# Kernel tuning notes

Hardware: AMD Instinct MI355X
Metric: run time of the kernel (lower is better)

Reference implementation:

```python
import jax, jax.numpy as jnp
import numpy as np

L, R, C = 4, 4, 32          # corr_levels, corr_radius, corr_channels
D = 2 * R + 1               # 9 displacements per axis
B, H, W = 2, 48, 64         # feature resolution (1/8 of a 384x512 image)


def _conv(x, w, b, stride=1, pad=1):
    out = jax.lax.conv_general_dilated(x, w, (stride, stride), [(pad, pad), (pad, pad)],
                                       dimension_numbers=('NCHW', 'OIHW', 'NCHW'))
    return out + b[None, :, None, None]


def _deconv(x, w, b):
    # ConvTranspose2d(k=4, s=2, p=1) as lhs-dilated conv with edge padding k-1-p = 2
    out = jax.lax.conv_general_dilated(x, w, (1, 1), [(2, 2), (2, 2)],
                                       lhs_dilation=(2, 2),
                                       dimension_numbers=('NCHW', 'OIHW', 'NCHW'))
    return out + b[None, :, None, None]


def _grid_sample(img, grid):
    # bilinear, align_corners=True, zero padding; img [B,C,H,W], grid [B,Hg,Wg,2] in [-1,1]
    Bn, Ch, Hi, Wi = img.shape
    gx = (grid[..., 0] + 1.0) * 0.5 * (Wi - 1)
    gy = (grid[..., 1] + 1.0) * 0.5 * (Hi - 1)
    x0 = jnp.floor(gx); y0 = jnp.floor(gy)
    wx = gx - x0; wy = gy - y0
    def corner(xi, yi, wgt):
        valid = (xi >= 0) & (xi <= Wi - 1) & (yi >= 0) & (yi <= Hi - 1)
        xc = jnp.clip(xi, 0, Wi - 1).astype(jnp.int32)
        yc = jnp.clip(yi, 0, Hi - 1).astype(jnp.int32)
        v = jax.vmap(lambda im, y, x: im[:, y, x])(img, yc, xc)  # [B,C,Hg,Wg]
        return v * (wgt * valid)[:, None, :, :]
    return (corner(x0, y0, (1 - wx) * (1 - wy)) + corner(x0 + 1, y0, wx * (1 - wy))
            + corner(x0, y0 + 1, (1 - wx) * wy) + corner(x0 + 1, y0 + 1, wx * wy))


def _mnet(x, w1, b1, w2, b2, w3, b3, w4, b4, w5, b5, w6, b6):
    # DICL matching net; eval-mode batchnorm with default stats is identity
    x = jax.nn.relu(_conv(x, w1, b1))
    x = jax.nn.relu(_conv(x, w2, b2, stride=2))
    x = jax.nn.relu(_conv(x, w3, b3))
    x = jax.nn.relu(_conv(x, w4, b4))
    x = jax.nn.relu(_deconv(x, w5, b5))
    return _conv(x, w6, b6)


def _forward(fmap1, fmap2, coords, mw1, mb1, mw2, mb2, mw3, mb3, mw4, mb4, mw5, mb5, mw6, mb6, dapw):
    Bn, _, h, w = coords.shape
    d = jnp.linspace(-R, R, D)
    # delta[i, j] = (dx[i], dy[j]) as in torch.meshgrid(indexing='ij')
    delta = jnp.stack(jnp.meshgrid(d, d, indexing='ij'), axis=-1).reshape(1, D, 1, D, 1, 2)
    cp = coords.transpose(0, 2, 3, 1).reshape(Bn, 1, h, 1, w, 2)
    out = []
    for i in range(L):
        f1, f2 = fmap1[i], fmap2[i]
        _, c, h2, w2 = f2.shape
        cen = cp / (2 ** i) + delta                          # [B,D,h,D,w,2]
        nx = 2.0 * cen[..., 0] / (w2 - 1) - 1.0
        ny = 2.0 * cen[..., 1] / (h2 - 1) - 1.0
        grid = jnp.stack([nx, ny], axis=-1).reshape(Bn, D * h, D * w, 2)
        f2s = _grid_sample(f2, grid).reshape(Bn, c, D, h, D, w).transpose(0, 2, 4, 1, 3, 5)
        f1b = jnp.broadcast_to(f1[:, None, None], (Bn, D, D, c, h, w))
        corr = jnp.concatenate([f1b, f2s], axis=3).reshape(Bn * D * D, 2 * c, h, w)
        cost = _mnet(corr, mw1[i], mb1[i], mw2[i], mb2[i], mw3[i], mb3[i],
                     mw4[i], mb4[i], mw5[i], mb5[i], mw6[i], mb6[i]).reshape(Bn, D * D, h, w)
        cost = jnp.einsum('oc,bchw->bohw', dapw[i], cost)    # DAP (1x1 conv, no bias)
        out.append(cost)
    return jnp.concatenate(out, axis=1)                      # [B, L*81, h, w]


def setup_inputs() -> dict:
    key = jax.random.key(0)
    ks = jax.random.split(key, 24)
    inp = {}
    for i in range(L):
        inp[f'fmap1_{i}'] = jax.random.normal(ks[i], (B, C, H, W), jnp.float32)
        inp[f'fmap2_{i}'] = jax.random.normal(ks[4 + i], (B, C, H >> i, W >> i), jnp.float32)
    ys, xs = jnp.meshgrid(jnp.arange(H, dtype=jnp.float32), jnp.arange(W, dtype=jnp.float32), indexing='ij')
    base = jnp.stack([xs, ys])[None]                          # [1,2,H,W]; ch0 = x, ch1 = y
    inp['coords'] = base + 4.0 * jax.random.normal(ks[8], (B, 2, H, W), jnp.float32)
    def he(k, shape):
        fan_in = shape[2] * shape[3] * shape[4]
        return jax.random.normal(k, shape, jnp.float32) * np.float32(np.sqrt(2.0 / fan_in))
    shapes = {'mw1': (L, 96, 2 * C, 3, 3), 'mw2': (L, 128, 96, 3, 3), 'mw3': (L, 128, 128, 3, 3),
              'mw4': (L, 64, 128, 3, 3), 'mw5': (L, 32, 64, 4, 4), 'mw6': (L, 1, 32, 3, 3)}
    for j, (name, s) in enumerate(shapes.items()):
        inp[name] = he(ks[9 + j], s)
        inp['mb' + name[2]] = jnp.zeros((L, s[1]), jnp.float32)
    eye = jnp.broadcast_to(jnp.eye(D * D, dtype=jnp.float32), (L, D * D, D * D))
    inp['dapw'] = eye + 0.01 * jax.random.normal(ks[20], (L, D * D, D * D), jnp.float32)
    return inp


def reference(fmap1_0, fmap1_1, fmap1_2, fmap1_3, fmap2_0, fmap2_1, fmap2_2, fmap2_3,
              coords, mw1, mb1, mw2, mb2, mw3, mb3, mw4, mb4, mw5, mb5, mw6, mb6, dapw):
    fmap1 = [fmap1_0, fmap1_1, fmap1_2, fmap1_3]
    fmap2 = [fmap2_0, fmap2_1, fmap2_2, fmap2_3]
    return _forward(fmap1, fmap2, coords, mw1, mb1, mw2, mb2, mw3, mb3,
                    mw4, mb4, mw5, mb5, mw6, mb6, dapw)
```

## Files before the change

### kernel.cpp

```cpp
#include <hip/hip_runtime.h>


typedef _Float16 half_t;
typedef _Float16 f16x8 __attribute__((ext_vector_type(8)));
typedef float f32x4 __attribute__((ext_vector_type(4)));

constexpr int D9 = 9, NB = 2, HH = 48, WW = 64;
constexpr int NIMG = NB * D9 * D9;
constexpr int HW = HH * WW;
constexpr int H2 = 24, W2 = 32, HW2 = H2 * W2;

constexpr int F1S = 9 * 1 * 6 * 512;
constexpr int F2S = 9 * 3 * 8 * 512;
constexpr int F3S = 9 * 4 * 8 * 512;
constexpr int F4S = 9 * 4 * 4 * 512;
constexpr int F5S = 4 * 4 * 2 * 2 * 512;
constexpr int KT1 = 576, WT1L = KT1 * 96;

static inline int cdiv(int a, int b) { return (a + b - 1) / b; }

__device__ __forceinline__ int xcd_swz(int b, int nb)
{
    int q = nb >> 3, r = nb & 7;
    int x = b & 7, j = b >> 3;
    return (x < r) ? (x * (q + 1) + j) : (r + x * q + j);
}

__global__ void transpose_w(const float* __restrict__ w, float* __restrict__ wT,
                            int OC, int K, int dstStride)
{
    int idx = blockIdx.x * blockDim.x + threadIdx.x;
    int tot = 4 * OC * K;
    if (idx >= tot) return;
    int lvl = idx / (OC * K);
    int r = idx - lvl * OC * K;
    int oc = r / K;
    int k = r - oc * K;
    wT[(size_t)lvl * dstStride + (size_t)k * OC + oc] = w[idx];
}

template <int OC, int ICSRC, int ICBASE, int ICS>
__global__ void prep3(const float* __restrict__ w, half_t* __restrict__ dst)
{
    constexpr int NT = OC / 16;
    constexpr int LS = 9 * ICS * NT * 512;
    int idx = blockIdx.x * blockDim.x + threadIdx.x;
    if (idx >= 4 * LS) return;
    int j = idx & 7, l = (idx >> 3) & 63;
    int r = idx >> 9;
    int tile = r % NT; r /= NT;
    int s = r % ICS;  r /= ICS;
    int t = r % 9;    r /= 9;
    int lvl = r;
    int ic = ICBASE + s * 32 + (l >> 4) * 8 + j;
    int oc = tile * 16 + (l & 15);
    float v = w[(size_t)lvl * OC * ICSRC * 9 + ((size_t)oc * ICSRC + ic) * 9 + t];
    dst[(size_t)lvl * LS + (((t * ICS + s) * NT + tile) << 9) + l * 8 + j] = (half_t)v;
}

__global__ void prep5(const float* __restrict__ w, half_t* __restrict__ dst)
{
    constexpr int LS = F5S;
    int idx = blockIdx.x * blockDim.x + threadIdx.x;
    if (idx >= 4 * LS) return;
    int j = idx & 7, l = (idx >> 3) & 63;
    int r = idx >> 9;
    int tile = r & 1; r >>= 1;
    int s = r & 1;    r >>= 1;
    int uv = r & 3;   r >>= 2;
    int cls = r & 3;  r >>= 2;
    int lvl = r;
    int u = uv >> 1, v = uv & 1, p = cls >> 1, q = cls & 1;
    int ky = p + 2 * u, kx = q + 2 * v;
    int ic = s * 32 + (l >> 4) * 8 + j;
    int oc = tile * 16 + (l & 15);
    float val = w[(size_t)lvl * 32 * 64 * 16 + ((size_t)oc * 64 + ic) * 16 + ky * 4 + kx];
    dst[(size_t)lvl * LS + (((cls * 8 + uv * 2 + s) * 2 + tile) << 9) + l * 8 + j] = (half_t)val;
}

__global__ __launch_bounds__(256)
void conv_part(const float* __restrict__ in, const float* __restrict__ wT,
               const float* __restrict__ bias, float* __restrict__ out)
{
    constexpr int TO = 16, IC = 32, OC = 96;
    int tx = threadIdx.x;
    int ox = tx % WW;
    int oy = blockIdx.x * 4 + tx / WW;
    int oc0 = blockIdx.y * TO;
    int n = blockIdx.z;

    float acc[TO];
    #pragma unroll
    for (int o = 0; o < TO; ++o) acc[o] = bias[oc0 + o];
    bool mL = ox >= 1, mR = ox + 1 < WW;
    int xl = mL ? ox - 1 : 0, xr = mR ? ox + 1 : WW - 1;
    const float* ip = in + (size_t)n * IC * HW;
    const float* wk = wT + oc0;
    for (int ic = 0; ic < IC; ++ic) {
        const float* icp = ip + ic * HW;
        const float* wpk = wk + ic * 9 * OC;
        #pragma unroll
        for (int ky = 0; ky < 3; ++ky) {
            int iy = oy + ky - 1;
            if ((unsigned)iy < (unsigned)HH) {
                const float* rp = icp + iy * WW;
                float v0 = rp[xl]; v0 = mL ? v0 : 0.f;
                float v1 = rp[ox];
                float v2 = rp[xr]; v2 = mR ? v2 : 0.f;
                const float* wp = wpk + ky * 3 * OC;
                #pragma unroll
                for (int o = 0; o < TO; ++o) acc[o] = fmaf(v0, wp[o], acc[o]);
                #pragma unroll
                for (int o = 0; o < TO; ++o) acc[o] = fmaf(v1, wp[OC + o], acc[o]);
                #pragma unroll
                for (int o = 0; o < TO; ++o) acc[o] = fmaf(v2, wp[2 * OC + o], acc[o]);
            }
        }
    }
    float* ob = out + ((size_t)n * HW + oy * WW + ox) * OC + oc0;
    #pragma unroll
    for (int o = 0; o < TO; ++o) ob[o] = acc[o];
}

__global__ void sample_kernel(const float* __restrict__ f2,
                              const float* __restrict__ coords, half_t* __restrict__ corr,
                              int n0, int nimg, int h2, int w2, float inv_scale)
{
    int idx = blockIdx.x * blockDim.x + threadIdx.x;
    if (idx >= nimg * HW) return;
    int x = idx % WW;
    int t = idx / WW;
    int y = t % HH;
    int nl = t / HH;
    int ng = n0 + nl;
    int b = ng / 81;
    int c81 = ng % 81;
    int di = c81 / D9, dj = c81 % D9;

    float cx = coords[((size_t)(b * 2 + 0) * HH + y) * WW + x];
    float cy = coords[((size_t)(b * 2 + 1) * HH + y) * WW + x];
    float gx = cx * inv_scale + (float)(di - 4);
    float gy = cy * inv_scale + (float)(dj - 4);
    float x0f = floorf(gx), y0f = floorf(gy);
    float wx = gx - x0f, wy = gy - y0f;
    int x0 = (int)x0f, y0 = (int)y0f;
    int x1 = x0 + 1, y1 = y0 + 1;
    bool vx0 = (x0 >= 0) && (x0 <= w2 - 1), vx1 = (x1 >= 0) && (x1 <= w2 - 1);
    bool vy0 = (y0 >= 0) && (y0 <= h2 - 1), vy1 = (y1 >= 0) && (y1 <= h2 - 1);
    int xc0 = min(max(x0, 0), w2 - 1), xc1 = min(max(x1, 0), w2 - 1);
    int yc0 = min(max(y0, 0), h2 - 1), yc1 = min(max(y1, 0), h2 - 1);
    float m00 = (vx0 && vy0) ? (1.f - wx) * (1.f - wy) : 0.f;
    float m10 = (vx1 && vy0) ? wx * (1.f - wy) : 0.f;
    float m01 = (vx0 && vy1) ? (1.f - wx) * wy : 0.f;
    float m11 = (vx1 && vy1) ? wx * wy : 0.f;

    const float* f2b = f2 + (size_t)b * 32 * h2 * w2;
    half_t* outb = corr + ((size_t)nl * HW + y * WW + x) * 32;
    int o00 = yc0 * w2 + xc0, o10 = yc0 * w2 + xc1;
    int o01 = yc1 * w2 + xc0, o11 = yc1 * w2 + xc1;
    #pragma unroll 8
    for (int ch = 0; ch < 32; ++ch) {
        const float* im = f2b + (size_t)ch * h2 * w2;
        float v = m00 * im[o00] + m10 * im[o10] + m01 * im[o01] + m11 * im[o11];
        outb[ch] = (half_t)v;
    }
}

template <int ICS, int ICT, int OC, int IH, int IW, int OH, int OW, int S, bool PARTI, int NTW>
__global__ __launch_bounds__(256)
void conv_mfma(const half_t* __restrict__ in, const half_t* __restrict__ wfrag,
               const float* __restrict__ bias, half_t* __restrict__ out,
               const float* __restrict__ part, int n0, int gx, int gxy, int nb)
{
    constexpr int NT = OC / 16;
    int lb = xcd_swz(blockIdx.x, nb);
    int n = lb / gxy;
    int rem = lb - n * gxy;
    int ty = rem / gx;
    int tx = rem - ty * gx;

    int lane = threadIdx.x & 63;
    int wv = threadIdx.x >> 6;
    int tile0 = ty * NTW;
    int pt0 = tx * 16 + wv * 4;
    int colc = lane & 15;
    int kg = lane >> 4;

    const half_t* inn = in + (size_t)n * IH * IW * ICT;

    int px[4], py[4];
    #pragma unroll
    for (int m = 0; m < 4; ++m) {
        int p = (pt0 + m) * 16 + colc;
        px[m] = p % OW;
        py[m] = p / OW;
    }

    f32x4 acc[4][NTW];
    if (PARTI) {
        int bimg = (n0 + n) / 81;
        const float* pp = part + (size_t)bimg * OH * OW * 96;
        #pragma unroll
        for (int m = 0; m < 4; ++m)
            #pragma unroll
            for (int nn = 0; nn < NTW; ++nn)
                #pragma unroll
                for (int j = 0; j < 4; ++j)
                    acc[m][nn][j] = pp[(size_t)((pt0 + m) * 16 + kg * 4 + j) * 96
                                       + (tile0 + nn) * 16 + colc];
    } else {
        #pragma unroll
        for (int nn = 0; nn < NTW; ++nn) {
            float bv = bias[(tile0 + nn) * 16 + colc];
            #pragma unroll
            for (int m = 0; m < 4; ++m)
                #pragma unroll
                for (int j = 0; j < 4; ++j) acc[m][nn][j] = bv;
        }
    }

    f16x8 zz = {};
    #pragma unroll
    for (int t = 0; t < 9; ++t) {
        int dy = t / 3 - 1, dx = t % 3 - 1;
        const half_t* ap[4];
        bool av[4];
        #pragma unroll
        for (int m = 0; m < 4; ++m) {
            int sx = px[m] * S + dx, sy = py[m] * S + dy;
            av[m] = ((unsigned)sx < (unsigned)IW) && ((unsigned)sy < (unsigned)IH);
            int sxc = min(max(sx, 0), IW - 1), syc = min(max(sy, 0), IH - 1);
            ap[m] = inn + ((size_t)syc * IW + sxc) * ICT + kg * 8;
        }
        #pragma unroll
        for (int s = 0; s < ICS; ++s) {
            f16x8 bv[NTW];
            #pragma unroll
            for (int nn = 0; nn < NTW; ++nn)
                bv[nn] = *(const f16x8*)(wfrag + (((t * ICS + s) * NT + tile0 + nn) << 9) + lane * 8);
            #pragma unroll
            for (int m = 0; m < 4; ++m) {
                f16x8 a = *(const f16x8*)(ap[m] + s * 32);
                a = av[m] ? a : zz;
                #pragma unroll
                for (int nn = 0; nn < NTW; ++nn)
                    acc[m][nn] = __builtin_amdgcn_mfma_f32_16x16x32_f16(a, bv[nn], acc[m][nn], 0, 0, 0);
            }
        }
    }

    #pragma unroll
    for (int m = 0; m < 4; ++m)
        #pragma unroll
        for (int nn = 0; nn < NTW; ++nn)
            #pragma unroll
            for (int j = 0; j < 4; ++j) {
                float r = fmaxf(acc[m][nn][j], 0.f);
                int p = (pt0 + m) * 16 + kg * 4 + j;
                out[((size_t)n * OH * OW + p) * OC + (tile0 + nn) * 16 + colc] = (half_t)r;
            }
}

__global__ __launch_bounds__(256)
void deconv_mfma(const half_t* __restrict__ in, const half_t* __restrict__ wfrag,
                 const float* __restrict__ bias, half_t* __restrict__ out, int nb)
{
    int lb = xcd_swz(blockIdx.x, nb);
    int n = lb / 12;
    int rem = lb - n * 12;
    int cls = rem / 3;
    int tx = rem - cls * 3;

    int lane = threadIdx.x & 63;
    int wv = threadIdx.x >> 6;
    int p = cls >> 1, q = cls & 1;
    int pt0 = tx * 16 + wv * 4;
    int colc = lane & 15, kg = lane >> 4;
    const half_t* inn = in + (size_t)n * HW2 * 64;

    int pa[4], pb[4];
    #pragma unroll
    for (int m = 0; m < 4; ++m) {
        int pos = (pt0 + m) * 16 + colc;
        pa[m] = pos >> 5;
        pb[m] = pos & 31;
    }

    f32x4 acc[4][2];
    float b0 = bias[colc], b1 = bias[16 + colc];
    #pragma unroll
    for (int m = 0; m < 4; ++m)
        #pragma unroll
        for (int j = 0; j < 4; ++j) { acc[m][0][j] = b0; acc[m][1][j] = b1; }

    f16x8 zz = {};
    #pragma unroll
    for (int uv = 0; uv < 4; ++uv) {
        int u = uv >> 1, v = uv & 1;
        const half_t* ap[4];
        bool av[4];
        #pragma unroll
        for (int m = 0; m < 4; ++m) {
            int sy = pa[m] + p - 1 + u, sx = pb[m] + q - 1 + v;
            av[m] = ((unsigned)sx < (unsigned)W2) && ((unsigned)sy < (unsigned)H2);
            int sxc = min(max(sx, 0), W2 - 1), syc = min(max(sy, 0), H2 - 1);
            ap[m] = inn + ((size_t)syc * W2 + sxc) * 64 + kg * 8;
        }
        #pragma unroll
        for (int s = 0; s < 2; ++s) {
            f16x8 b0v = *(const f16x8*)(wfrag + (((cls * 8 + uv * 2 + s) * 2 + 0) << 9) + lane * 8);
            f16x8 b1v = *(const f16x8*)(wfrag + (((cls * 8 + uv * 2 + s) * 2 + 1) << 9) + lane * 8);
            #pragma unroll
            for (int m = 0; m < 4; ++m) {
                f16x8 a = *(const f16x8*)(ap[m] + s * 32);
                a = av[m] ? a : zz;
                acc[m][0] = __builtin_amdgcn_mfma_f32_16x16x32_f16(a, b0v, acc[m][0], 0, 0, 0);
                acc[m][1] = __builtin_amdgcn_mfma_f32_16x16x32_f16(a, b1v, acc[m][1], 0, 0, 0);
            }
        }
    }

    #pragma unroll
    for (int m = 0; m < 4; ++m)
        #pragma unroll
        for (int nn = 0; nn < 2; ++nn)
            #pragma unroll
            for (int j = 0; j < 4; ++j) {
                int pos = (pt0 + m) * 16 + kg * 4 + j;
                int a2 = pos >> 5, b2 = pos & 31;
                int oy = 2 * a2 + p, ox = 2 * b2 + q;
                float r = fmaxf(acc[m][nn][j], 0.f);
                out[((size_t)n * HW + oy * WW + ox) * 32 + nn * 16 + colc] = (half_t)r;
            }
}

__global__ void conv6_kernel(const half_t* __restrict__ in, const float* __restrict__ w6,
                             const float* __restrict__ b6, float* __restrict__ cost,
                             int n0, int nimg)
{
    int idx = blockIdx.x * blockDim.x + threadIdx.x;
    if (idx >= nimg * HW) return;
    int x = idx % WW;
    int t = idx / WW;
    int y = t % HH;
    int nl = t / HH;
    float acc = b6[0];
    const half_t* ib = in + (size_t)nl * HW * 32;
    #pragma unroll
    for (int tap = 0; tap < 9; ++tap) {
        int sy = y + tap / 3 - 1, sx = x + tap % 3 - 1;
        if ((unsigned)sy < (unsigned)HH && (unsigned)sx < (unsigned)WW) {
            const f16x8* pp = (const f16x8*)(ib + ((size_t)sy * WW + sx) * 32);
            #pragma unroll
            for (int c8 = 0; c8 < 4; ++c8) {
                f16x8 v = pp[c8];
                #pragma unroll
                for (int j = 0; j < 8; ++j)
                    acc = fmaf((float)v[j], w6[(c8 * 8 + j) * 9 + tap], acc);
            }
        }
    }
    cost[(size_t)(n0 + nl) * HW + y * WW + x] = acc;
}

__global__ void dap_kernel(const float* __restrict__ cost, const float* __restrict__ dapw,
                           float* __restrict__ out, int lvl)
{
    int idx = blockIdx.x * blockDim.x + threadIdx.x;
    if (idx >= NB * 81 * HW) return;
    int px = idx % HW;
    int t = idx / HW;
    int o = t % 81;
    int b = t / 81;
    const float* dw = dapw + (size_t)o * 81;
    const float* cb = cost + (size_t)b * 81 * HW + px;
    float acc = 0.f;
    #pragma unroll 9
    for (int c = 0; c < 81; ++c) acc = fmaf(dw[c], cb[(size_t)c * HW], acc);
    out[((size_t)(b * 4 * 81 + lvl * 81 + o)) * HW + px] = acc;
}

extern "C" void kernel_launch(void* const* d_in, const int* in_sizes, int n_in,
                              void* d_out, int out_size, void* d_ws, size_t ws_size,
                              hipStream_t stream)
{
    const float* f1[4] = {(const float*)d_in[0], (const float*)d_in[2],
                          (const float*)d_in[4], (const float*)d_in[6]};
    const float* f2[4] = {(const float*)d_in[1], (const float*)d_in[3],
                          (const float*)d_in[5], (const float*)d_in[7]};
    const float* coords = (const float*)d_in[8];
    const float* mw1 = (const float*)d_in[9];
    const float* mb1 = (const float*)d_in[10];
    const float* mw2 = (const float*)d_in[11];
    const float* mb2 = (const float*)d_in[12];
    const float* mw3 = (const float*)d_in[13];
    const float* mb3 = (const float*)d_in[14];
    const float* mw4 = (const float*)d_in[15];
    const float* mb4 = (const float*)d_in[16];
    const float* mw5 = (const float*)d_in[17];
    const float* mb5 = (const float*)d_in[18];
    const float* mw6 = (const float*)d_in[19];
    const float* mb6 = (const float*)d_in[20];
    const float* dapw = (const float*)d_in[21];
    float* out = (float*)d_out;

    auto al = [](size_t x) { return (x + 255) / 256 * 256; };
    const size_t wT1B = al((size_t)4 * WT1L * 4);
    const size_t fragB = al((size_t)4 * (F1S + F2S + F3S + F4S + F5S) * 2);
    const size_t partB = al((size_t)NB * HW * 96 * 4);
    const size_t costB = al((size_t)NIMG * HW * 4);
    const size_t SA = (size_t)HW * 32 * 2;
    const size_t SB = (size_t)HW * 96 * 2;

    static const int divs[10] = {162, 81, 54, 27, 18, 9, 6, 3, 2, 1};
    int chunk = 1;
    for (int i = 0; i < 10; ++i) {
        size_t need = wT1B + fragB + partB + costB + (size_t)divs[i] * (SA + SB) + 1024;
        if (need <= ws_size) { chunk = divs[i]; break; }
    }

    char* wsb = (char*)d_ws;
    float* wT1 = (float*)wsb;
    half_t* frags = (half_t*)(wsb + wT1B);
    half_t* Fr1 = frags;
    half_t* Fr2 = Fr1 + (size_t)4 * F1S;
    half_t* Fr3 = Fr2 + (size_t)4 * F2S;
    half_t* Fr4 = Fr3 + (size_t)4 * F3S;
    half_t* Fr5 = Fr4 + (size_t)4 * F4S;
    float* part = (float*)(wsb + wT1B + fragB);
    float* cost = (float*)(wsb + wT1B + fragB + partB);
    half_t* bufA = (half_t*)(wsb + wT1B + fragB + partB + costB);
    half_t* bufB = (half_t*)(wsb + wT1B + fragB + partB + costB + (size_t)chunk * SA);

    const int TPB = 256;

    transpose_w<<<cdiv(4 * 96 * KT1, TPB), TPB, 0, stream>>>(mw1, wT1, 96, KT1, WT1L);
    prep3<96, 64, 32, 1><<<cdiv(4 * F1S, TPB), TPB, 0, stream>>>(mw1, Fr1);
    prep3<128, 96, 0, 3><<<cdiv(4 * F2S, TPB), TPB, 0, stream>>>(mw2, Fr2);
    prep3<128, 128, 0, 4><<<cdiv(4 * F3S, TPB), TPB, 0, stream>>>(mw3, Fr3);
    prep3<64, 128, 0, 4><<<cdiv(4 * F4S, TPB), TPB, 0, stream>>>(mw4, Fr4);
    prep5<<<cdiv(4 * F5S, TPB), TPB, 0, stream>>>(mw5, Fr5);

    for (int lvl = 0; lvl < 4; ++lvl) {
        int h2 = HH >> lvl, w2 = WW >> lvl;
        float inv_scale = 1.0f / (float)(1 << lvl);
        const float* b1 = mb1 + (size_t)lvl * 96;
        const float* b2 = mb2 + (size_t)lvl * 128;
        const float* b3 = mb3 + (size_t)lvl * 128;
        const float* b4 = mb4 + (size_t)lvl * 64;
        const float* b5 = mb5 + (size_t)lvl * 32;
        const float* w6 = mw6 + (size_t)lvl * 288;
        const float* b6 = mb6 + (size_t)lvl * 1;

        conv_part<<<dim3(12, 6, 2), TPB, 0, stream>>>(f1[lvl], wT1 + (size_t)lvl * WT1L, b1, part);

        for (int n0 = 0; n0 < NIMG; n0 += chunk) {
            int n = chunk;
            sample_kernel<<<cdiv(n * HW, TPB), TPB, 0, stream>>>(
                f2[lvl], coords, bufA, n0, n, h2, w2, inv_scale);
            { int gx = 12, gxy = 24, nb = gxy * n;
              conv_mfma<1, 32, 96, 48, 64, 48, 64, 1, true, 3><<<nb, TPB, 0, stream>>>(
                  bufA, Fr1 + (size_t)lvl * F1S, b1, bufB, part, n0, gx, gxy, nb); }
            { int gx = 3, gxy = 6, nb = gxy * n;
              conv_mfma<3, 96, 128, 48, 64, 24, 32, 2, false, 4><<<nb, TPB, 0, stream>>>(
                  bufB, Fr2 + (size_t)lvl * F2S, b2, bufA, nullptr, 0, gx, gxy, nb); }
            { int gx = 3, gxy = 6, nb = gxy * n;
              conv_mfma<4, 128, 128, 24, 32, 24, 32, 1, false, 4><<<nb, TPB, 0, stream>>>(
                  bufA, Fr3 + (size_t)lvl * F3S, b3, bufB, nullptr, 0, gx, gxy, nb); }
            { int gx = 3, gxy = 3, nb = gxy * n;
              conv_mfma<4, 128, 64, 24, 32, 24, 32, 1, false, 4><<<nb, TPB, 0, stream>>>(
                  bufB, Fr4 + (size_t)lvl * F4S, b4, bufA, nullptr, 0, gx, gxy, nb); }
            { int nb = 12 * n;
              deconv_mfma<<<nb, TPB, 0, stream>>>(bufA, Fr5 + (size_t)lvl * F5S, b5, bufB, nb); }
            conv6_kernel<<<cdiv(n * HW, TPB), TPB, 0, stream>>>(bufB, w6, b6, cost, n0, n);
        }
        dap_kernel<<<cdiv(NB * 81 * HW, TPB), TPB, 0, stream>>>(
            cost, dapw + (size_t)lvl * 81 * 81, out, lvl);
    }
}
```

Before: 1.908 ms.

## Batch all four pyramid levels into single launches and halve per-block tile width

Removes the per-level host loop so every stage (conv_part, sampling, the matching-net convs, deconv, conv6, DAP) covers all four levels in one grid, with each block deriving its level from the global image index. The chunk-size options grow to allow up to 648 images per pass, so there are fewer launches and larger grids. The per-block output tile count (NTW) drops from 3/4 to 2, doubling block counts to raise occupancy. The cost is larger workspace buffers and more index arithmetic per thread.

```diff
diff --git a/kernel.cpp b/kernel.cpp
--- a/kernel.cpp
+++ b/kernel.cpp
@@ -7,6 +7,7 @@
 
 constexpr int D9 = 9, NB = 2, HH = 48, WW = 64;
 constexpr int NIMG = NB * D9 * D9;
+constexpr int NTOT = 4 * NIMG;
 constexpr int HW = HH * WW;
 constexpr int H2 = 24, W2 = 32, HW2 = H2 * W2;
 
@@ -79,25 +80,32 @@
 }
 
 __global__ __launch_bounds__(256)
-void conv_part(const float* __restrict__ in, const float* __restrict__ wT,
-               const float* __restrict__ bias, float* __restrict__ out)
+void conv_part(const float* __restrict__ f1_0, const float* __restrict__ f1_1,
+               const float* __restrict__ f1_2, const float* __restrict__ f1_3,
+               const float* __restrict__ wT1, const float* __restrict__ mb1,
+               float* __restrict__ part)
 {
     constexpr int TO = 16, IC = 32, OC = 96;
+    int z = blockIdx.z;
+    int lvl = z >> 1, b = z & 1;
+    const float* in = (lvl == 0 ? f1_0 : lvl == 1 ? f1_1 : lvl == 2 ? f1_2 : f1_3)
+                      + (size_t)b * IC * HW;
+    const float* wT = wT1 + (size_t)lvl * WT1L;
+    const float* bias = mb1 + lvl * 96;
+
     int tx = threadIdx.x;
     int ox = tx % WW;
     int oy = blockIdx.x * 4 + tx / WW;
     int oc0 = blockIdx.y * TO;
-    int n = blockIdx.z;
 
     float acc[TO];
     #pragma unroll
     for (int o = 0; o < TO; ++o) acc[o] = bias[oc0 + o];
     bool mL = ox >= 1, mR = ox + 1 < WW;
     int xl = mL ? ox - 1 : 0, xr = mR ? ox + 1 : WW - 1;
-    const float* ip = in + (size_t)n * IC * HW;
     const float* wk = wT + oc0;
     for (int ic = 0; ic < IC; ++ic) {
-        const float* icp = ip + ic * HW;
+        const float* icp = in + ic * HW;
         const float* wpk = wk + ic * 9 * OC;
         #pragma unroll
         for (int ky = 0; ky < 3; ++ky) {
@@ -117,14 +125,15 @@
             }
         }
     }
-    float* ob = out + ((size_t)n * HW + oy * WW + ox) * OC + oc0;
+    float* ob = part + ((size_t)z * HW + oy * WW + ox) * OC + oc0;
     #pragma unroll
     for (int o = 0; o < TO; ++o) ob[o] = acc[o];
 }
 
-__global__ void sample_kernel(const float* __restrict__ f2,
+__global__ void sample_kernel(const float* __restrict__ f2_0, const float* __restrict__ f2_1,
+                              const float* __restrict__ f2_2, const float* __restrict__ f2_3,
                               const float* __restrict__ coords, half_t* __restrict__ corr,
-                              int n0, int nimg, int h2, int w2, float inv_scale)
+                              int n0, int nimg)
 {
     int idx = blockIdx.x * blockDim.x + threadIdx.x;
     if (idx >= nimg * HW) return;
@@ -132,10 +141,15 @@
     int t = idx / WW;
     int y = t % HH;
     int nl = t / HH;
-    int ng = n0 + nl;
-    int b = ng / 81;
-    int c81 = ng % 81;
+    int g = n0 + nl;
+    int lvl = g / NIMG;
+    int i = g - lvl * NIMG;
+    int b = i / 81;
+    int c81 = i - b * 81;
     int di = c81 / D9, dj = c81 % D9;
+    const float* f2 = (lvl == 0 ? f2_0 : lvl == 1 ? f2_1 : lvl == 2 ? f2_2 : f2_3);
+    int h2 = HH >> lvl, w2 = WW >> lvl;
+    float inv_scale = 1.0f / (float)(1 << lvl);
 
     float cx = coords[((size_t)(b * 2 + 0) * HH + y) * WW + x];
     float cy = coords[((size_t)(b * 2 + 1) * HH + y) * WW + x];
@@ -168,8 +182,8 @@
 
 template <int ICS, int ICT, int OC, int IH, int IW, int OH, int OW, int S, bool PARTI, int NTW>
 __global__ __launch_bounds__(256)
-void conv_mfma(const half_t* __restrict__ in, const half_t* __restrict__ wfrag,
-               const float* __restrict__ bias, half_t* __restrict__ out,
+void conv_mfma(const half_t* __restrict__ in, const half_t* __restrict__ fragBase, int FS,
+               const float* __restrict__ biasBase, half_t* __restrict__ out,
                const float* __restrict__ part, int n0, int gx, int gxy, int nb)
 {
     constexpr int NT = OC / 16;
@@ -178,6 +192,10 @@
     int rem = lb - n * gxy;
     int ty = rem / gx;
     int tx = rem - ty * gx;
+    int g = n0 + n;
+    int lvl = g / NIMG;
+    const half_t* wfrag = fragBase + (size_t)lvl * FS;
+    const float* bias = biasBase + lvl * OC;
 
     int lane = threadIdx.x & 63;
     int wv = threadIdx.x >> 6;
@@ -198,8 +216,9 @@
 
     f32x4 acc[4][NTW];
     if (PARTI) {
-        int bimg = (n0 + n) / 81;
-        const float* pp = part + (size_t)bimg * OH * OW * 96;
+        int i = g - lvl * NIMG;
+        int pimg = lvl * 2 + i / 81;
+        const float* pp = part + (size_t)pimg * OH * OW * 96;
         #pragma unroll
         for (int m = 0; m < 4; ++m)
             #pragma unroll
@@ -262,14 +281,18 @@
 }
 
 __global__ __launch_bounds__(256)
-void deconv_mfma(const half_t* __restrict__ in, const half_t* __restrict__ wfrag,
-                 const float* __restrict__ bias, half_t* __restrict__ out, int nb)
+void deconv_mfma(const half_t* __restrict__ in, const half_t* __restrict__ fragBase,
+                 const float* __restrict__ mb5, half_t* __restrict__ out, int n0, int nb)
 {
     int lb = xcd_swz(blockIdx.x, nb);
     int n = lb / 12;
     int rem = lb - n * 12;
     int cls = rem / 3;
     int tx = rem - cls * 3;
+    int g = n0 + n;
+    int lvl = g / NIMG;
+    const half_t* wfrag = fragBase + (size_t)lvl * F5S;
+    const float* bias = mb5 + lvl * 32;
 
     int lane = threadIdx.x & 63;
     int wv = threadIdx.x >> 6;
@@ -334,8 +357,8 @@
             }
 }
 
-__global__ void conv6_kernel(const half_t* __restrict__ in, const float* __restrict__ w6,
-                             const float* __restrict__ b6, float* __restrict__ cost,
+__global__ void conv6_kernel(const half_t* __restrict__ in, const float* __restrict__ mw6,
+                             const float* __restrict__ mb6, float* __restrict__ cost,
                              int n0, int nimg)
 {
     int idx = blockIdx.x * blockDim.x + threadIdx.x;
@@ -344,7 +367,10 @@
     int t = idx / WW;
     int y = t % HH;
     int nl = t / HH;
-    float acc = b6[0];
+    int g = n0 + nl;
+    int lvl = g / NIMG;
+    const float* w6 = mw6 + (size_t)lvl * 288;
+    float acc = mb6[lvl];
     const half_t* ib = in + (size_t)nl * HW * 32;
     #pragma unroll
     for (int tap = 0; tap < 9; ++tap) {
@@ -360,34 +386,40 @@
             }
         }
     }
-    cost[(size_t)(n0 + nl) * HW + y * WW + x] = acc;
+    cost[(size_t)g * HW + y * WW + x] = acc;
 }
 
 __global__ void dap_kernel(const float* __restrict__ cost, const float* __restrict__ dapw,
-                           float* __restrict__ out, int lvl)
-{
-    int idx = blockIdx.x * blockDim.x + threadIdx.x;
-    if (idx >= NB * 81 * HW) return;
+                           float* __restrict__ out)
+{
+    int idx = blockIdx.x * blockDim.x + threadIdx.x;
+    if (idx >= 4 * NB * 81 * HW) return;
     int px = idx % HW;
     int t = idx / HW;
     int o = t % 81;
-    int b = t / 81;
-    const float* dw = dapw + (size_t)o * 81;
-    const float* cb = cost + (size_t)b * 81 * HW + px;
+    t /= 81;
+    int b = t & 1;
+    int lvl = t >> 1;
+    const float* dw = dapw + (size_t)lvl * 6561 + (size_t)o * 81;
+    const float* cb = cost + ((size_t)lvl * NIMG + b * 81) * HW + px;
     float acc = 0.f;
     #pragma unroll 9
     for (int c = 0; c < 81; ++c) acc = fmaf(dw[c], cb[(size_t)c * HW], acc);
-    out[((size_t)(b * 4 * 81 + lvl * 81 + o)) * HW + px] = acc;
+    out[((size_t)(b * 324 + lvl * 81 + o)) * HW + px] = acc;
 }
 
 extern "C" void kernel_launch(void* const* d_in, const int* in_sizes, int n_in,
                               void* d_out, int out_size, void* d_ws, size_t ws_size,
                               hipStream_t stream)
 {
-    const float* f1[4] = {(const float*)d_in[0], (const float*)d_in[2],
-                          (const float*)d_in[4], (const float*)d_in[6]};
-    const float* f2[4] = {(const float*)d_in[1], (const float*)d_in[3],
-                          (const float*)d_in[5], (const float*)d_in[7]};
+    const float* f1_0 = (const float*)d_in[0];
+    const float* f2_0 = (const float*)d_in[1];
+    const float* f1_1 = (const float*)d_in[2];
+    const float* f2_1 = (const float*)d_in[3];
+    const float* f1_2 = (const float*)d_in[4];
+    const float* f2_2 = (const float*)d_in[5];
+    const float* f1_3 = (const float*)d_in[6];
+    const float* f2_3 = (const float*)d_in[7];
     const float* coords = (const float*)d_in[8];
     const float* mw1 = (const float*)d_in[9];
     const float* mb1 = (const float*)d_in[10];
@@ -407,14 +439,14 @@
     auto al = [](size_t x) { return (x + 255) / 256 * 256; };
     const size_t wT1B = al((size_t)4 * WT1L * 4);
     const size_t fragB = al((size_t)4 * (F1S + F2S + F3S + F4S + F5S) * 2);
-    const size_t partB = al((size_t)NB * HW * 96 * 4);
-    const size_t costB = al((size_t)NIMG * HW * 4);
+    const size_t partB = al((size_t)8 * HW * 96 * 4);
+    const size_t costB = al((size_t)NTOT * HW * 4);
     const size_t SA = (size_t)HW * 32 * 2;
     const size_t SB = (size_t)HW * 96 * 2;
 
-    static const int divs[10] = {162, 81, 54, 27, 18, 9, 6, 3, 2, 1};
+    static const int divs[12] = {648, 324, 216, 162, 108, 81, 54, 36, 27, 18, 9, 1};
     int chunk = 1;
-    for (int i = 0; i < 10; ++i) {
+    for (int i = 0; i < 12; ++i) {
         size_t need = wT1B + fragB + partB + costB + (size_t)divs[i] * (SA + SB) + 1024;
         if (need <= ws_size) { chunk = divs[i]; break; }
     }
@@ -441,40 +473,27 @@
     prep3<64, 128, 0, 4><<<cdiv(4 * F4S, TPB), TPB, 0, stream>>>(mw4, Fr4);
     prep5<<<cdiv(4 * F5S, TPB), TPB, 0, stream>>>(mw5, Fr5);
 
-    for (int lvl = 0; lvl < 4; ++lvl) {
-        int h2 = HH >> lvl, w2 = WW >> lvl;
-        float inv_scale = 1.0f / (float)(1 << lvl);
-        const float* b1 = mb1 + (size_t)lvl * 96;
-        const float* b2 = mb2 + (size_t)lvl * 128;
-        const float* b3 = mb3 + (size_t)lvl * 128;
-        const float* b4 = mb4 + (size_t)lvl * 64;
-        const float* b5 = mb5 + (size_t)lvl * 32;
-        const float* w6 = mw6 + (size_t)lvl * 288;
-        const float* b6 = mb6 + (size_t)lvl * 1;
-
-        conv_part<<<dim3(12, 6, 2), TPB, 0, stream>>>(f1[lvl], wT1 + (size_t)lvl * WT1L, b1, part);
-
-        for (int n0 = 0; n0 < NIMG; n0 += chunk) {
-            int n = chunk;
-            sample_kernel<<<cdiv(n * HW, TPB), TPB, 0, stream>>>(
-                f2[lvl], coords, bufA, n0, n, h2, w2, inv_scale);
-            { int gx = 12, gxy = 24, nb = gxy * n;
-              conv_mfma<1, 32, 96, 48, 64, 48, 64, 1, true, 3><<<nb, TPB, 0, stream>>>(
-                  bufA, Fr1 + (size_t)lvl * F1S, b1, bufB, part, n0, gx, gxy, nb); }
-            { int gx = 3, gxy = 6, nb = gxy * n;
-              conv_mfma<3, 96, 128, 48, 64, 24, 32, 2, false, 4><<<nb, TPB, 0, stream>>>(
-                  bufB, Fr2 + (size_t)lvl * F2S, b2, bufA, nullptr, 0, gx, gxy, nb); }
-            { int gx = 3, gxy = 6, nb = gxy * n;
-              conv_mfma<4, 128, 128, 24, 32, 24, 32, 1, false, 4><<<nb, TPB, 0, stream>>>(
-                  bufA, Fr3 + (size_t)lvl * F3S, b3, bufB, nullptr, 0, gx, gxy, nb); }
-            { int gx = 3, gxy = 3, nb = gxy * n;
-              conv_mfma<4, 128, 64, 24, 32, 24, 32, 1, false, 4><<<nb, TPB, 0, stream>>>(
-                  bufB, Fr4 + (size_t)lvl * F4S, b4, bufA, nullptr, 0, gx, gxy, nb); }
-            { int nb = 12 * n;
-              deconv_mfma<<<nb, TPB, 0, stream>>>(bufA, Fr5 + (size_t)lvl * F5S, b5, bufB, nb); }
-            conv6_kernel<<<cdiv(n * HW, TPB), TPB, 0, stream>>>(bufB, w6, b6, cost, n0, n);
-        }
-        dap_kernel<<<cdiv(NB * 81 * HW, TPB), TPB, 0, stream>>>(
-            cost, dapw + (size_t)lvl * 81 * 81, out, lvl);
-    }
-}
+    conv_part<<<dim3(12, 6, 8), TPB, 0, stream>>>(f1_0, f1_1, f1_2, f1_3, wT1, mb1, part);
+
+    for (int n0 = 0; n0 < NTOT; n0 += chunk) {
+        int n = chunk;
+        sample_kernel<<<cdiv(n * HW, TPB), TPB, 0, stream>>>(
+            f2_0, f2_1, f2_2, f2_3, coords, bufA, n0, n);
+        { int gx = 12, gxy = 36, nb = gxy * n;
+          conv_mfma<1, 32, 96, 48, 64, 48, 64, 1, true, 2><<<nb, TPB, 0, stream>>>(
+              bufA, Fr1, F1S, mb1, bufB, part, n0, gx, gxy, nb); }
+        { int gx = 3, gxy = 12, nb = gxy * n;
+          conv_mfma<3, 96, 128, 48, 64, 24, 32, 2, false, 2><<<nb, TPB, 0, stream>>>(
+              bufB, Fr2, F2S, mb2, bufA, nullptr, n0, gx, gxy, nb); }
+        { int gx = 3, gxy = 12, nb = gxy * n;
+          conv_mfma<4, 128, 128, 24, 32, 24, 32, 1, false, 2><<<nb, TPB, 0, stream>>>(
+              bufA, Fr3, F3S, mb3, bufB, nullptr, n0, gx, gxy, nb); }
+        { int gx = 3, gxy = 6, nb = gxy * n;
+          conv_mfma<4, 128, 64, 24, 32, 24, 32, 1, false, 2><<<nb, TPB, 0, stream>>>(
+              bufB, Fr4, F4S, mb4, bufA, nullptr, n0, gx, gxy, nb); }
+        { int nb = 12 * n;
+          deconv_mfma<<<nb, TPB, 0, stream>>>(bufA, Fr5, mb5, bufB, n0, nb); }
+        conv6_kernel<<<cdiv(n * HW, TPB), TPB, 0, stream>>>(bufB, mw6, mb6, cost, n0, n);
+    }
+    dap_kernel<<<cdiv(4 * NB * 81 * HW, TPB), TPB, 0, stream>>>(cost, dapw, out);
+}
```

After: 2.424 ms. +27.1%, slower.
